# Optimization experiments

Measured on AMD Instinct MI355X. Metric: run time of the kernel, lower is better.

## Reference

```python
import jax, jax.numpy as jnp
import numpy as np

SOFT_MATCH_THRESHOLD = 0.1
EPSILON = 1e-8
SOFT_JACCARD_WEIGHT = 1.0
MSE_MZ_WEIGHT = 1.0
MSE_INTENSITY_WEIGHT = 1.0
SIGN_PENALTY_WEIGHT = 1.0

BATCH, SEQ = 32, 2048


def setup_inputs() -> dict:
    key = jax.random.key(0)
    k1, k2, k3, k4 = jax.random.split(key, 4)
    shape = (BATCH, SEQ)
    return {
        "pred_mz": jax.random.normal(k1, shape, dtype=jnp.float32),
        "mz": jax.random.normal(k2, shape, dtype=jnp.float32),
        "intensity": jax.random.normal(k3, shape, dtype=jnp.float32),
        "pred_intensity": jax.random.normal(k4, shape, dtype=jnp.float32),
    }


def _soft_jaccard_loss(pred_mz, mz, pred_intensity):
    pred_mask = pred_mz >= 0
    true_mask = mz >= 0
    pred_mz = jnp.where(pred_mask, pred_mz, 0.0)
    pred_intensity = jnp.where(pred_mask, pred_intensity, 0.0)
    mz = jnp.where(true_mask, mz, 0.0)
    # [B, S, S] pairwise |pred_mz_i - mz_j|
    mz_diff = jnp.abs(pred_mz[:, :, None] - mz[:, None, :])
    soft_match = jnp.max(jnp.exp(-mz_diff / SOFT_MATCH_THRESHOLD), axis=2)  # [B, S]
    soft_intersect = jnp.sum(soft_match * pred_intensity, axis=1)  # [B]
    soft_union = pred_mask.sum(axis=1) + true_mask.sum(axis=1)  # [B]
    soft_jaccard = (soft_intersect + EPSILON) / (soft_union + EPSILON)
    return jnp.mean(1.0 - soft_jaccard)


def _mse_loss(pred_mz, mz, pred_intensity, intensity):
    loss_mz = jnp.mean((pred_mz - mz) ** 2)
    loss_intensity = jnp.mean((pred_intensity - intensity) ** 2)
    max_mz = jnp.max(jnp.abs(mz))
    max_intensity = jnp.max(jnp.abs(intensity))
    return loss_mz / max_mz ** 2, loss_intensity / max_intensity ** 2


def _sign_penalty(pred_mz, mz, pred_intensity, intensity):
    p_mz = jnp.mean(jnp.abs(jnp.sign(pred_mz) - jnp.sign(mz)))
    p_int = jnp.mean(jnp.abs(jnp.sign(pred_intensity) - jnp.sign(intensity)))
    return (p_mz + p_int) / 2.0


def reference(pred_mz, mz, intensity, pred_intensity):
    sj = _soft_jaccard_loss(pred_mz, mz, pred_intensity)
    loss_mz, loss_intensity = _mse_loss(pred_mz, mz, pred_intensity, intensity)
    sp = _sign_penalty(pred_mz, mz, pred_intensity, intensity)
    return (
        SOFT_JACCARD_WEIGHT * sj,
        MSE_MZ_WEIGHT * loss_mz,
        MSE_INTENSITY_WEIGHT * loss_intensity,
        SIGN_PENALTY_WEIGHT * sp,
    )
```

## Files before the change

kernel.cpp:

```cpp
#include <hip/hip_runtime.h>

#define S 2048
#define B 32
#define NEPS 1e-8f

__device__ __forceinline__ float sgnf(float x) {
    return (x > 0.f ? 1.f : 0.f) - (x < 0.f ? 1.f : 0.f);
}

__global__ __launch_bounds__(256, 4) void loss_main(
    const float* __restrict__ pred_mz, const float* __restrict__ mz,
    const float* __restrict__ intensity, const float* __restrict__ pred_intensity,
    float* __restrict__ ws)
{
    __shared__ __align__(16) float smz[S];
    __shared__ float smin[4][64];

    const int blk   = blockIdx.x;
    const int b     = blk >> 5;
    const int chunk = blk & 31;
    const int tid   = threadIdx.x;
    const int lane  = tid & 63;
    const int w     = tid >> 6;

    const float* mzrow = mz + b * S;

    {
        const float4* g4 = (const float4*)mzrow;
        float4* l4 = (float4*)smz;
        #pragma unroll
        for (int r = 0; r < 2; ++r) {
            int k = tid + 256 * r;
            float4 v = g4[k];
            v.x = (v.x >= 0.f) ? v.x : 0.f;
            v.y = (v.y >= 0.f) ? v.y : 0.f;
            v.z = (v.z >= 0.f) ? v.z : 0.f;
            v.w = (v.w >= 0.f) ? v.w : 0.f;
            l4[k] = v;
        }
    }
    __syncthreads();

    const int i   = chunk * 64 + lane;
    const int gi  = b * S + i;
    const float pmz = pred_mz[gi];
    const float a   = (pmz >= 0.f) ? pmz : 0.f;

    float m0 = 1e30f, m1 = 1e30f, m2 = 1e30f, m3 = 1e30f;
    const float4* s4 = (const float4*)smz + w * 128;
    #pragma unroll 4
    for (int j = 0; j < 128; ++j) {
        float4 v = s4[j];
        m0 = fminf(m0, fabsf(a - v.x));
        m1 = fminf(m1, fabsf(a - v.y));
        m2 = fminf(m2, fabsf(a - v.z));
        m3 = fminf(m3, fabsf(a - v.w));
    }
    smin[w][lane] = fminf(fminf(m0, m1), fminf(m2, m3));
    __syncthreads();

    if (tid < 64) {
        float mind = fminf(fminf(smin[0][lane], smin[1][lane]),
                           fminf(smin[2][lane], smin[3][lane]));
        float sm = exp2f(mind * -14.426950408889634f);

        const float tmz = mzrow[i];
        const float pin = pred_intensity[gi];
        const float tin = intensity[gi];

        float vals[6];
        vals[0] = (pmz >= 0.f) ? sm * pin : 0.f;
        vals[1] = (pmz >= 0.f ? 1.f : 0.f) + (tmz >= 0.f ? 1.f : 0.f);
        float d0 = pmz - tmz; vals[2] = d0 * d0;
        float d1 = pin - tin; vals[3] = d1 * d1;
        vals[4] = fabsf(sgnf(pmz) - sgnf(tmz));
        vals[5] = fabsf(sgnf(pin) - sgnf(tin));
        float vmax0 = fabsf(tmz);
        float vmax1 = fabsf(tin);

        #pragma unroll
        for (int off = 32; off; off >>= 1) {
            #pragma unroll
            for (int k = 0; k < 6; ++k) vals[k] += __shfl_down(vals[k], off, 64);
            vmax0 = fmaxf(vmax0, __shfl_down(vmax0, off, 64));
            vmax1 = fmaxf(vmax1, __shfl_down(vmax1, off, 64));
        }
        if (lane == 0) {
            float* p = ws + blk * 8;
            p[0] = vals[0]; p[1] = vals[1]; p[2] = vals[2]; p[3] = vals[3];
            p[4] = vals[4]; p[5] = vals[5]; p[6] = vmax0;   p[7] = vmax1;
        }
    }
}

__global__ __launch_bounds__(256) void loss_finalize(const float* __restrict__ ws,
                                                     float* __restrict__ out)
{
    __shared__ float red[4][7];
    const int t    = threadIdx.x;
    const int lane = t & 63;
    const int w    = t >> 6;

    float I = 0.f, U = 0.f, s2 = 0.f, s3 = 0.f, s4 = 0.f, s5 = 0.f;
    float mx0 = 0.f, mx1 = 0.f;
    #pragma unroll
    for (int k = 0; k < 4; ++k) {
        const float* p = ws + (t * 4 + k) * 8;
        I  += p[0]; U  += p[1];
        s2 += p[2]; s3 += p[3];
        s4 += p[4]; s5 += p[5];
        mx0 = fmaxf(mx0, p[6]); mx1 = fmaxf(mx1, p[7]);
    }
    #pragma unroll
    for (int off = 4; off; off >>= 1) {
        I += __shfl_down(I, off, 8);
        U += __shfl_down(U, off, 8);
    }
    float jl = ((t & 7) == 0) ? (1.f - (I + NEPS) / (U + NEPS)) : 0.f;

    #pragma unroll
    for (int off = 32; off; off >>= 1) {
        jl += __shfl_down(jl, off, 64);
        s2 += __shfl_down(s2, off, 64);
        s3 += __shfl_down(s3, off, 64);
        s4 += __shfl_down(s4, off, 64);
        s5 += __shfl_down(s5, off, 64);
        mx0 = fmaxf(mx0, __shfl_down(mx0, off, 64));
        mx1 = fmaxf(mx1, __shfl_down(mx1, off, 64));
    }
    if (lane == 0) {
        red[w][0] = jl; red[w][1] = s2; red[w][2] = s3;
        red[w][3] = s4; red[w][4] = s5; red[w][5] = mx0; red[w][6] = mx1;
    }
    __syncthreads();
    if (t == 0) {
        float fjl = red[0][0], f2 = red[0][1], f3 = red[0][2], f4 = red[0][3],
              f5 = red[0][4], fm0 = red[0][5], fm1 = red[0][6];
        #pragma unroll
        for (int wv = 1; wv < 4; ++wv) {
            fjl += red[wv][0]; f2 += red[wv][1]; f3 += red[wv][2];
            f4  += red[wv][3]; f5 += red[wv][4];
            fm0 = fmaxf(fm0, red[wv][5]); fm1 = fmaxf(fm1, red[wv][6]);
        }
        const float inv_n = 1.0f / (float)(B * S);
        out[0] = fjl / (float)B;
        out[1] = (f2 * inv_n) / (fm0 * fm0);
        out[2] = (f3 * inv_n) / (fm1 * fm1);
        out[3] = (f4 + f5) * inv_n * 0.5f;
    }
}

extern "C" void kernel_launch(void* const* d_in, const int* in_sizes, int n_in,
                              void* d_out, int out_size, void* d_ws, size_t ws_size,
                              hipStream_t stream) {
    const float* pred_mz        = (const float*)d_in[0];
    const float* mz             = (const float*)d_in[1];
    const float* intensity      = (const float*)d_in[2];
    const float* pred_intensity = (const float*)d_in[3];
    float* out = (float*)d_out;
    float* ws  = (float*)d_ws;

    loss_main<<<B * 32, 256, 0, stream>>>(pred_mz, mz, intensity, pred_intensity, ws);
    loss_finalize<<<1, 256, 0, stream>>>(ws, out);
}
```

Baseline: 14.35 us.

## Process two query rows per thread to halve blocks and reuse LDS loads

Each block now handles 128 predicted m/z values instead of 64, with every thread comparing two query values against each LDS-loaded float4, so the grid shrinks from 1024 to 512 blocks. This halves the redundant per-block staging of the mz row into shared memory and doubles arithmetic per LDS read. The epilogue now reduces across all four waves through shared memory, writes the partials as float4, and the finalize kernel reads 512 partials with float4 loads. The cost is fewer blocks, higher register pressure (launch bounds relaxed to 2 blocks per SM), and an extra barrier-plus-shared-memory reduction.

```diff
diff --git a/kernel.cpp b/kernel.cpp
--- a/kernel.cpp
+++ b/kernel.cpp
@@ -8,17 +8,18 @@
     return (x > 0.f ? 1.f : 0.f) - (x < 0.f ? 1.f : 0.f);
 }
 
-__global__ __launch_bounds__(256, 4) void loss_main(
+__global__ __launch_bounds__(256, 2) void loss_main(
     const float* __restrict__ pred_mz, const float* __restrict__ mz,
     const float* __restrict__ intensity, const float* __restrict__ pred_intensity,
     float* __restrict__ ws)
 {
     __shared__ __align__(16) float smz[S];
-    __shared__ float smin[4][64];
+    __shared__ float smin[4][128];
+    __shared__ float red[4][8];
 
     const int blk   = blockIdx.x;
-    const int b     = blk >> 5;
-    const int chunk = blk & 31;
+    const int b     = blk >> 4;
+    const int chunk = blk & 15;
     const int tid   = threadIdx.x;
     const int lane  = tid & 63;
     const int w     = tid >> 6;
@@ -41,55 +42,82 @@
     }
     __syncthreads();
 
-    const int i   = chunk * 64 + lane;
-    const int gi  = b * S + i;
-    const float pmz = pred_mz[gi];
-    const float a   = (pmz >= 0.f) ? pmz : 0.f;
+    const int i0  = chunk * 128 + lane;
+    const int gi0 = b * S + i0;
+    const float p0 = pred_mz[gi0];
+    const float p1 = pred_mz[gi0 + 64];
+    const float a0 = (p0 >= 0.f) ? p0 : 0.f;
+    const float a1 = (p1 >= 0.f) ? p1 : 0.f;
 
-    float m0 = 1e30f, m1 = 1e30f, m2 = 1e30f, m3 = 1e30f;
+    float m00 = 1e30f, m01 = 1e30f, m10 = 1e30f, m11 = 1e30f;
     const float4* s4 = (const float4*)smz + w * 128;
-    #pragma unroll 4
+    #pragma unroll 8
     for (int j = 0; j < 128; ++j) {
         float4 v = s4[j];
-        m0 = fminf(m0, fabsf(a - v.x));
-        m1 = fminf(m1, fabsf(a - v.y));
-        m2 = fminf(m2, fabsf(a - v.z));
-        m3 = fminf(m3, fabsf(a - v.w));
+        float d0 = a0 - v.x, d1 = a0 - v.y, d2 = a0 - v.z, d3 = a0 - v.w;
+        m00 = fminf(fminf(m00, fabsf(d0)), fabsf(d1));
+        m01 = fminf(fminf(m01, fabsf(d2)), fabsf(d3));
+        float e0 = a1 - v.x, e1 = a1 - v.y, e2 = a1 - v.z, e3 = a1 - v.w;
+        m10 = fminf(fminf(m10, fabsf(e0)), fabsf(e1));
+        m11 = fminf(fminf(m11, fabsf(e2)), fabsf(e3));
     }
-    smin[w][lane] = fminf(fminf(m0, m1), fminf(m2, m3));
+    smin[w][lane]      = fminf(m00, m01);
+    smin[w][lane + 64] = fminf(m10, m11);
     __syncthreads();
 
-    if (tid < 64) {
-        float mind = fminf(fminf(smin[0][lane], smin[1][lane]),
-                           fminf(smin[2][lane], smin[3][lane]));
+    float vals[6] = {0.f, 0.f, 0.f, 0.f, 0.f, 0.f};
+    float vmax0 = 0.f, vmax1 = 0.f;
+    if (tid < 128) {
+        float mind = fminf(fminf(smin[0][tid], smin[1][tid]),
+                           fminf(smin[2][tid], smin[3][tid]));
         float sm = exp2f(mind * -14.426950408889634f);
 
+        const int i  = chunk * 128 + tid;
+        const int gi = b * S + i;
+        const float pmz = pred_mz[gi];
         const float tmz = mzrow[i];
         const float pin = pred_intensity[gi];
         const float tin = intensity[gi];
 
-        float vals[6];
         vals[0] = (pmz >= 0.f) ? sm * pin : 0.f;
         vals[1] = (pmz >= 0.f ? 1.f : 0.f) + (tmz >= 0.f ? 1.f : 0.f);
         float d0 = pmz - tmz; vals[2] = d0 * d0;
         float d1 = pin - tin; vals[3] = d1 * d1;
         vals[4] = fabsf(sgnf(pmz) - sgnf(tmz));
         vals[5] = fabsf(sgnf(pin) - sgnf(tin));
-        float vmax0 = fabsf(tmz);
-        float vmax1 = fabsf(tin);
+        vmax0 = fabsf(tmz);
+        vmax1 = fabsf(tin);
+    }
 
+    #pragma unroll
+    for (int off = 32; off; off >>= 1) {
         #pragma unroll
-        for (int off = 32; off; off >>= 1) {
+        for (int k = 0; k < 6; ++k) vals[k] += __shfl_down(vals[k], off, 64);
+        vmax0 = fmaxf(vmax0, __shfl_down(vmax0, off, 64));
+        vmax1 = fmaxf(vmax1, __shfl_down(vmax1, off, 64));
+    }
+    if (lane == 0) {
+        #pragma unroll
+        for (int k = 0; k < 6; ++k) red[w][k] = vals[k];
+        red[w][6] = vmax0;
+        red[w][7] = vmax1;
+    }
+    __syncthreads();
+
+    if (tid == 0) {
+        float s[8];
+        #pragma unroll
+        for (int k = 0; k < 8; ++k) s[k] = red[0][k];
+        #pragma unroll
+        for (int wv = 1; wv < 4; ++wv) {
             #pragma unroll
-            for (int k = 0; k < 6; ++k) vals[k] += __shfl_down(vals[k], off, 64);
-            vmax0 = fmaxf(vmax0, __shfl_down(vmax0, off, 64));
-            vmax1 = fmaxf(vmax1, __shfl_down(vmax1, off, 64));
+            for (int k = 0; k < 6; ++k) s[k] += red[wv][k];
+            s[6] = fmaxf(s[6], red[wv][6]);
+            s[7] = fmaxf(s[7], red[wv][7]);
         }
-        if (lane == 0) {
-            float* p = ws + blk * 8;
-            p[0] = vals[0]; p[1] = vals[1]; p[2] = vals[2]; p[3] = vals[3];
-            p[4] = vals[4]; p[5] = vals[5]; p[6] = vmax0;   p[7] = vmax1;
-        }
+        float4* p = (float4*)(ws + blk * 8);
+        p[0] = make_float4(s[0], s[1], s[2], s[3]);
+        p[1] = make_float4(s[4], s[5], s[6], s[7]);
     }
 }
 
@@ -104,12 +132,13 @@
     float I = 0.f, U = 0.f, s2 = 0.f, s3 = 0.f, s4 = 0.f, s5 = 0.f;
     float mx0 = 0.f, mx1 = 0.f;
     #pragma unroll
-    for (int k = 0; k < 4; ++k) {
-        const float* p = ws + (t * 4 + k) * 8;
-        I  += p[0]; U  += p[1];
-        s2 += p[2]; s3 += p[3];
-        s4 += p[4]; s5 += p[5];
-        mx0 = fmaxf(mx0, p[6]); mx1 = fmaxf(mx1, p[7]);
+    for (int k = 0; k < 2; ++k) {
+        const float4* p = (const float4*)(ws + (t * 2 + k) * 8);
+        float4 lo = p[0], hi = p[1];
+        I  += lo.x; U  += lo.y;
+        s2 += lo.z; s3 += lo.w;
+        s4 += hi.x; s5 += hi.y;
+        mx0 = fmaxf(mx0, hi.z); mx1 = fmaxf(mx1, hi.w);
     }
     #pragma unroll
     for (int off = 4; off; off >>= 1) {
@@ -160,6 +189,6 @@
     float* out = (float*)d_out;
     float* ws  = (float*)d_ws;
 
-    loss_main<<<B * 32, 256, 0, stream>>>(pred_mz, mz, intensity, pred_intensity, ws);
+    loss_main<<<B * 16, 256, 0, stream>>>(pred_mz, mz, intensity, pred_intensity, ws);
     loss_finalize<<<1, 256, 0, stream>>>(ws, out);
 }
```

After: 15.42 us, median of 2. 7.5% more time.
